# Kernel optimization log

Hardware: AMD Instinct MI355X
Metric: run time of the kernel (lower is better)

## Reference

```python
import math
import jax, jax.numpy as jnp
import numpy as np

# ---- config (from ModelConfig) ----
HIDDEN = 2880
HEAD_DIM = 64
N_HEADS = 64
N_KV = 8
Q_MULT = N_HEADS // N_KV  # 8
SLIDING_WINDOW = 128      # left context; causal windowed attention
ROPE_BASE = 150000.0
ROPE_SCALE = 32.0
NTK_ALPHA = 1.0
NTK_BETA = 32.0
INIT_CTX = 4096
RMS_EPS = 1e-5
SM_SCALE = 1.0 / math.sqrt(HEAD_DIM)
Q_DIM = N_HEADS * HEAD_DIM   # 4096
KV_DIM = N_KV * HEAD_DIM     # 512
QKV_DIM = Q_DIM + 2 * KV_DIM # 5120
B, T = 1, 2048


def _rope_cos_sin(n_tokens):
    """YaRN-scaled rotary cache, per RotaryEmbedding._compute_concentration_and_inv_freq."""
    d_half = HEAD_DIM // 2
    freq = ROPE_BASE ** (jnp.arange(0, HEAD_DIM, 2, dtype=jnp.float32) / HEAD_DIM)
    concentration = 0.1 * math.log(ROPE_SCALE) + 1.0
    low = d_half * math.log(INIT_CTX / (NTK_BETA * 2 * math.pi)) / math.log(ROPE_BASE)
    high = d_half * math.log(INIT_CTX / (NTK_ALPHA * 2 * math.pi)) / math.log(ROPE_BASE)
    interpolation = 1.0 / (ROPE_SCALE * freq)
    extrapolation = 1.0 / freq
    ramp = (jnp.arange(d_half, dtype=jnp.float32) - low) / (high - low)
    mask = 1.0 - jnp.clip(ramp, 0.0, 1.0)
    inv_freq = interpolation * (1.0 - mask) + extrapolation * mask
    pos = jnp.arange(n_tokens, dtype=jnp.float32)
    angles = pos[:, None] * inv_freq[None, :]  # [t, d/2]
    return jnp.cos(angles) * concentration, jnp.sin(angles) * concentration


def _apply_rope(x, cos, sin):
    """Interleaved RoPE (matches _apply_rotary_emb). x: [b, t, ..., d]."""
    shape = x.shape
    n_mid = x.ndim - 3  # dims between token axis and feature axis
    c = cos.reshape((1, shape[1]) + (1,) * n_mid + (shape[-1] // 2,))
    s = sin.reshape((1, shape[1]) + (1,) * n_mid + (shape[-1] // 2,))
    x1 = x[..., ::2]
    x2 = x[..., 1::2]
    o1 = x1 * c - x2 * s
    o2 = x2 * c + x1 * s
    return jnp.stack((o1, o2), axis=-1).reshape(shape)


def _rmsnorm(x, scale):
    t = x.astype(jnp.float32)
    t = t * jax.lax.rsqrt(jnp.mean(t * t, axis=-1, keepdims=True) + RMS_EPS)
    return (t * scale).astype(x.dtype)


def setup_inputs() -> dict:
    key = jax.random.key(0)
    ks = jax.random.split(key, 7)
    x = jax.random.normal(ks[0], (B, T, HIDDEN), dtype=jnp.float32)
    norm_scale = jnp.ones((HIDDEN,), dtype=jnp.float32)
    w_qkv = jax.random.normal(ks[1], (QKV_DIM, HIDDEN), dtype=jnp.float32) * (HIDDEN ** -0.5)
    b_qkv = jax.random.normal(ks[2], (QKV_DIM,), dtype=jnp.float32) * 0.02
    sinks = jax.random.normal(ks[3], (N_HEADS,), dtype=jnp.float32)
    w_out = jax.random.normal(ks[4], (HIDDEN, Q_DIM), dtype=jnp.float32) * (Q_DIM ** -0.5)
    b_out = jax.random.normal(ks[5], (HIDDEN,), dtype=jnp.float32) * 0.02
    return {"x": x, "norm_scale": norm_scale, "w_qkv": w_qkv, "b_qkv": b_qkv,
            "sinks": sinks, "w_out": w_out, "b_out": b_out}


def reference(x, norm_scale, w_qkv, b_qkv, sinks, w_out, b_out):
    b, t, _ = x.shape
    h = _rmsnorm(x, norm_scale)
    qkv = h @ w_qkv.T + b_qkv  # [b, t, 5120]
    q = qkv[..., :Q_DIM].reshape(b, t, N_KV, Q_MULT, HEAD_DIM)
    k = qkv[..., Q_DIM:Q_DIM + KV_DIM].reshape(b, t, N_KV, HEAD_DIM)
    v = qkv[..., Q_DIM + KV_DIM:].reshape(b, t, N_KV, HEAD_DIM)

    cos, sin = _rope_cos_sin(t)
    q = _apply_rope(q, cos, sin)
    k = _apply_rope(k, cos, sin)

    # sliding-window causal attention with sink logits (sdpa windowed path)
    left_ctx = SLIDING_WINDOW
    window = left_ctx + 1
    kp = jnp.pad(k, ((0, 0), (left_ctx, 0), (0, 0), (0, 0)))
    vp = jnp.pad(v, ((0, 0), (left_ctx, 0), (0, 0), (0, 0)))
    gather_idx = jnp.arange(t)[:, None] + jnp.arange(window)[None, :]  # into padded axis
    kwin = kp[:, gather_idx]  # [b, t, w, n_kv, d]
    vwin = vp[:, gather_idx]

    pos = jnp.arange(t)[:, None] + (jnp.arange(window) - left_ctx)[None, :]
    valid = (pos >= 0) & (pos < t)  # [t, w]

    scores = jnp.einsum('bthqd,btwhd->bthqw', q, kwin).astype(jnp.float32) * SM_SCALE
    scores = jnp.where(valid[None, :, None, None, :], scores, -jnp.inf)

    sink = (sinks * math.log(2.0)).reshape(N_KV, Q_MULT)
    sink = jnp.broadcast_to(sink[None, None, :, :, None], (b, t, N_KV, Q_MULT, 1))
    scores = jnp.concatenate([scores, sink], axis=-1)  # [b, t, h, q, w+1]

    w_attn = jax.nn.softmax(scores, axis=-1)[..., :-1].astype(v.dtype)
    attn = jnp.einsum('bthqw,btwhd->bthqd', w_attn, vwin).reshape(b, t, -1)

    out = attn @ w_out.T + b_out
    return x + out
```

## Files before the change

kernel.cpp:

```cpp
#include <hip/hip_runtime.h>
#include <math.h>

typedef unsigned short u16;
typedef unsigned int   u32;
using f32x4  = __attribute__((ext_vector_type(4))) float;
using bf16x8 = __attribute__((ext_vector_type(8))) __bf16;

#define HIDDEN   2880
#define QKVD     5120
#define QD       4096
#define TTOK     2048
#define NKV      8
#define QMULT    8
#define HD       64
#define NPAD     2944

#define PREP_QKV_BLOCKS  14400
#define PREP_RMS_BLOCKS  2048

static __device__ __forceinline__ float bflo(u32 u){ return __uint_as_float(u << 16); }
static __device__ __forceinline__ float bfhi(u32 u){ return __uint_as_float(u & 0xffff0000u); }
static __device__ __forceinline__ u16 f2bf(float f){
    u32 u = __float_as_uint(f);
    u32 r = (u + 0x7fffu + ((u >> 16) & 1u)) >> 16;
    return (u16)r;
}

static __device__ __forceinline__ void glds16(const void* g, void* l) {
    __builtin_amdgcn_global_load_lds(
        (__attribute__((address_space(1))) void*)g,
        (__attribute__((address_space(3))) void*)l,
        16, 0, 0);
}

#define BARB()  __builtin_amdgcn_s_barrier()
#define SB0()   __builtin_amdgcn_sched_barrier(0)
#define LGKM0() do { asm volatile("s_waitcnt lgkmcnt(0)"); SB0(); } while (0)
#define VMW(N)  do { SB0(); asm volatile("s_waitcnt vmcnt(" #N ")"); SB0(); } while (0)

__global__ __launch_bounds__(256) void prep_kernel(const float* __restrict__ w_qkv,
                                                   u16* __restrict__ wqkv_bf,
                                                   const float* __restrict__ x,
                                                   const float* __restrict__ scale,
                                                   u16* __restrict__ h) {
    const int b = blockIdx.x;
    const int tid = threadIdx.x;
    if (b < PREP_QKV_BLOCKS) {
        int i = b * 256 + tid;
        float4 f = ((const float4*)w_qkv)[i];
        ushort4 o;
        o.x = f2bf(f.x); o.y = f2bf(f.y); o.z = f2bf(f.z); o.w = f2bf(f.w);
        ((ushort4*)wqkv_bf)[i] = o;
    } else {
        const int t = b - PREP_QKV_BLOCKS;
        const float4* xr = (const float4*)(x + (long)t * HIDDEN);
        float4 v[3];
        float ss = 0.f;
        #pragma unroll
        for (int it = 0; it < 3; ++it) {
            int i4 = tid + it * 256;
            if (i4 < 720) {
                v[it] = xr[i4];
                ss += v[it].x*v[it].x + v[it].y*v[it].y + v[it].z*v[it].z + v[it].w*v[it].w;
            }
        }
        #pragma unroll
        for (int off = 32; off > 0; off >>= 1) ss += __shfl_down(ss, off);
        __shared__ float red[4];
        if ((tid & 63) == 0) red[tid >> 6] = ss;
        __syncthreads();
        float tot = red[0] + red[1] + red[2] + red[3];
        float rr = rsqrtf(tot * (1.0f / HIDDEN) + 1e-5f);
        ushort4* hr = (ushort4*)(h + (long)t * HIDDEN);
        #pragma unroll
        for (int it = 0; it < 3; ++it) {
            int i4 = tid + it * 256;
            if (i4 < 720) {
                float4 s4 = ((const float4*)scale)[i4];
                ushort4 o;
                o.x = f2bf(v[it].x * rr * s4.x);
                o.y = f2bf(v[it].y * rr * s4.y);
                o.z = f2bf(v[it].z * rr * s4.z);
                o.w = f2bf(v[it].w * rr * s4.w);
                hr[i4] = o;
            }
        }
    }
}


#define LOAD_AQ(MH) do { \
    aq[0][0] = *(const bf16x8*)(aS + (2*(MH)+0)*2048 + off0); \
    aq[0][1] = *(const bf16x8*)(aS + (2*(MH)+0)*2048 + off1); \
    aq[1][0] = *(const bf16x8*)(aS + (2*(MH)+1)*2048 + off0); \
    aq[1][1] = *(const bf16x8*)(aS + (2*(MH)+1)*2048 + off1); \
} while (0)

#define MFMA_Q(MH) do { \
    __builtin_amdgcn_s_setprio(1); \
    _Pragma("unroll") \
    for (int i2_ = 0; i2_ < 2; ++i2_) { \
        _Pragma("unroll") \
        for (int ni_ = 0; ni_ < 4; ++ni_) { \
            acc[2*(MH)+i2_][ni_] = __builtin_amdgcn_mfma_f32_16x16x32_bf16(aq[i2_][0], bq[ni_][0], acc[2*(MH)+i2_][ni_], 0, 0, 0); \
            acc[2*(MH)+i2_][ni_] = __builtin_amdgcn_mfma_f32_16x16x32_bf16(aq[i2_][1], bq[ni_][1], acc[2*(MH)+i2_][ni_], 0, 0, 0); \
        } \
    } \
    __builtin_amdgcn_s_setprio(0); \
} while (0)

__global__ __launch_bounds__(512, 2) void gemm_bt_8ph(const u16* __restrict__ A,
                                                      const u16* __restrict__ B,
                                                      u16* __restrict__ C0,
                                                      int N, int K, int ksplit,
                                                      int blimit, int colmax,
                                                      int nz_gemm,
                                                      const float* __restrict__ wout_src,
                                                      u16* __restrict__ wout_dst) {
    const int tid  = threadIdx.x;

    if ((int)blockIdx.z >= nz_gemm) {
        const long nb = (long)gridDim.x * gridDim.y;
        long bidx = (long)blockIdx.y * gridDim.x + blockIdx.x;
        long i = bidx * 512 + tid;
        const long tot = (long)NPAD * QD / 4;
        const long stride = nb * 512;
        for (; i < tot; i += stride) {
            long idx = i * 4;
            int row = (int)(idx >> 12);
            int col = (int)(idx & 4095);
            ushort4 o;
            if (row < HIDDEN) {
                float4 f = *(const float4*)(wout_src + (long)row * QD + col);
                o.x = f2bf(f.x); o.y = f2bf(f.y); o.z = f2bf(f.z); o.w = f2bf(f.w);
            } else {
                o.x = 0; o.y = 0; o.z = 0; o.w = 0;
            }
            ((ushort4*)wout_dst)[i] = o;
        }
        return;
    }

    extern __shared__ u16 smem[];
    u16* const smA = smem;
    u16* const smB = smem + 3 * 256 * 64;
    const int lane = tid & 63;
    const int wv   = tid >> 6;
    const int wm   = wv >> 2;
    const int wn   = wv & 3;
    const long m0  = (long)blockIdx.y * 256;
    const long n0  = (long)blockIdx.x * 256;
    const int kbase = blockIdx.z * ksplit;
    int krem = K - kbase; if (krem > ksplit) krem = ksplit;
    const int NT   = krem >> 6;
    u16* C = C0 + (size_t)blockIdx.z * ((size_t)TTOK * N);

    const int srow = tid >> 3;
    const int sg8  = ((tid & 7) ^ (srow & 7)) << 3;
    const int fr   = lane & 15;
    const int off0 = ((lane >> 4) << 4) ^ ((lane & 7) << 4);
    const int off1 = off0 ^ 64;
    const char* aR = (const char*)smA + (wm * 128 + fr) * 128;
    const char* bR = (const char*)smB + (wn * 64  + fr) * 128;

    f32x4 acc[8][4];
    #pragma unroll
    for (int i = 0; i < 8; ++i)
        #pragma unroll
        for (int j = 0; j < 4; ++j) acc[i][j] = f32x4{0.f, 0.f, 0.f, 0.f};

    const u16* Asrc = A + (m0 + srow) * (long)K + kbase + sg8;
    auto stageA = [&](int t, int slot) {
        char* dst = (char*)smA + slot * 32768 + (wv * 8) * 128;
        const u16* src = Asrc + t * 64;
        #pragma unroll
        for (int hj = 0; hj < 4; ++hj)
            glds16(src + (size_t)(hj * 64) * K, dst + hj * 64 * 128);
    };
    auto stageB = [&](int t, int h) {
        char* dst = (char*)smB + (t & 1) * 32768 + (h * 128 + wv * 8) * 128;
        #pragma unroll
        for (int j = 0; j < 2; ++j) {
            long r = n0 + h * 128 + j * 64 + srow;
            if (r > blimit) r = blimit;
            glds16(B + (size_t)r * K + kbase + t * 64 + sg8, dst + j * 64 * 128);
        }
    };

    stageA(0, 0);
    stageB(0, 0); stageB(0, 1);
    if (NT > 1) {
        stageA(1, 1); stageB(1, 0); stageB(1, 1);
        VMW(8);
    } else {
        VMW(0);
    }
    BARB();

    int sA = 0;
    for (int t = 0; t < NT; ++t) {
        const char* aS = aR + sA * 32768;
        const char* bS = bR + (t & 1) * 32768;
        int sA2 = sA + 2; if (sA2 >= 3) sA2 -= 3;
        bf16x8 bq[4][2], aq[2][2];
        #pragma unroll
        for (int ni = 0; ni < 4; ++ni) {
            bq[ni][0] = *(const bf16x8*)(bS + ni * 2048 + off0);
            bq[ni][1] = *(const bf16x8*)(bS + ni * 2048 + off1);
        }
        LOAD_AQ(0);
        if (t + 2 < NT) stageA(t + 2, sA2);
        BARB();
        LGKM0();
        MFMA_Q(0);
        BARB();
        LOAD_AQ(1);
        if (t + 2 < NT) stageB(t + 2, 0);
        BARB();
        LGKM0();
        MFMA_Q(1);
        BARB();
        LOAD_AQ(2);
        if (t + 2 < NT) stageB(t + 2, 1);
        BARB();
        LGKM0();
        MFMA_Q(2);
        BARB();
        LOAD_AQ(3);
        BARB();
        LGKM0();
        MFMA_Q(3);
        if (t + 2 < NT)      VMW(8);
        else if (t + 1 < NT) VMW(0);
        BARB();
        sA = (sA == 2) ? 0 : sA + 1;
    }

    const int cr = (lane >> 4) * 4;
    const int cc = lane & 15;
    #pragma unroll
    for (int ni = 0; ni < 4; ++ni) {
        long col = n0 + wn * 64 + ni * 16 + cc;
        if (col < colmax) {
            #pragma unroll
            for (int mi = 0; mi < 8; ++mi) {
                long row = m0 + wm * 128 + mi * 16 + cr;
                #pragma unroll
                for (int r2 = 0; r2 < 4; ++r2)
                    C[(row + r2) * (long)N + col] = f2bf(acc[mi][ni][r2]);
            }
        }
    }
}

__global__ __launch_bounds__(256) void rope_kernel(const u16* __restrict__ p1,
                                                   const float* __restrict__ b_qkv,
                                                   u16* __restrict__ qr,
                                                   u16* __restrict__ kr,
                                                   u16* __restrict__ vr,
                                                   int nsplit) {
    const int t = blockIdx.x;
    const int tid = threadIdx.x;
    __shared__ float cs[32], sn[32];
    if (tid < 32) {
        float fi = (float)tid;
        float freq   = exp2f(17.1946032f * (fi * (1.0f / 32.0f)));
        float interp = 1.0f / (32.0f * freq);
        float extra  = 1.0f / freq;
        float ramp   = (fi - 8.0927802f) * (1.0f / (17.3980220f - 8.0927802f));
        float rc     = fminf(fmaxf(ramp, 0.0f), 1.0f);
        float invf   = interp * rc + extra * (1.0f - rc);
        float ang    = (float)t * invf;
        cs[tid] = cosf(ang) * 1.3465736f;
        sn[tid] = sinf(ang) * 1.3465736f;
    }
    __syncthreads();
    const u16* rowA = p1 + (long)t * QKVD;
    auto pair = [&](int col) -> float2 {
        float2 bb = *(const float2*)(b_qkv + col);
        float a = bb.x, b = bb.y;
        for (int s = 0; s < nsplit; ++s) {
            u32 u = *(const u32*)(rowA + (size_t)s * TTOK * QKVD + col);
            a += bflo(u); b += bfhi(u);
        }
        return make_float2(a, b);
    };
    for (int p = tid; p < 2048; p += 256) {
        int hd2 = p >> 5, i = p & 31;
        float2 ab = pair(hd2 * 64 + 2 * i);
        float o1 = ab.x * cs[i] - ab.y * sn[i];
        float o2 = ab.y * cs[i] + ab.x * sn[i];
        *(u32*)(qr + (long)t * QD + hd2 * 64 + 2 * i) = (u32)f2bf(o1) | ((u32)f2bf(o2) << 16);
    }
    {
        int kv = tid >> 5, i = tid & 31;
        float2 ab = pair(QD + kv * 64 + 2 * i);
        float o1 = ab.x * cs[i] - ab.y * sn[i];
        float o2 = ab.y * cs[i] + ab.x * sn[i];
        *(u32*)(kr + ((long)kv * TTOK + t) * HD + 2 * i) = (u32)f2bf(o1) | ((u32)f2bf(o2) << 16);
    }
    {
        int kv = tid >> 5, d2 = tid & 31;
        float2 ab = pair(QD + 512 + kv * 64 + 2 * d2);
        *(u32*)(vr + ((long)kv * TTOK + t) * HD + 2 * d2) = (u32)f2bf(ab.x) | ((u32)f2bf(ab.y) << 16);
    }
}

__global__ __launch_bounds__(256, 2) void attn_kernel(const u16* __restrict__ qr,
                                                      const u16* __restrict__ kr,
                                                      const u16* __restrict__ vr,
                                                      const float* __restrict__ sinks,
                                                      u16* __restrict__ o) {
    const int t0  = blockIdx.x * 16;
    const int h   = blockIdx.y;
    const int qhg = blockIdx.z;
    const int tid = threadIdx.x;
    const int lane = tid & 63, wv = tid >> 6;
    __shared__ __align__(16) u16 ks[144][72];
    __shared__ __align__(16) u16 Vt[64][168];
    __shared__ __align__(16) u16 P [4][16][168];
    const u16* kb = kr + (long)h * TTOK * HD;
    const u16* vb = vr + (long)h * TTOK * HD;

    #pragma unroll
    for (int i = 0; i < 5; ++i) {
        int idx = i * 256 + tid;
        if (idx < 144 * 8) {
            int rr = idx >> 3, c = idx & 7;
            int tk = t0 - 128 + rr;
            int tks = tk < 0 ? 0 : tk;
            *(uint4*)&ks[rr][c * 8] = *(const uint4*)(kb + (long)tks * HD + c * 8);
        }
    }
    #pragma unroll
    for (int c4 = 0; c4 < 8; ++c4) {
        if (tid < 144) {
            int tk = t0 - 128 + tid;
            int tks = tk < 0 ? 0 : tk;
            uint4 v4 = *(const uint4*)(vb + (long)tks * HD + c4 * 8);
            int d0 = c4 * 8;
            Vt[d0+0][tid] = (u16)(v4.x & 0xffff); Vt[d0+1][tid] = (u16)(v4.x >> 16);
            Vt[d0+2][tid] = (u16)(v4.y & 0xffff); Vt[d0+3][tid] = (u16)(v4.y >> 16);
            Vt[d0+4][tid] = (u16)(v4.z & 0xffff); Vt[d0+5][tid] = (u16)(v4.z >> 16);
            Vt[d0+6][tid] = (u16)(v4.w & 0xffff); Vt[d0+7][tid] = (u16)(v4.w >> 16);
        }
    }
    if (tid < 128) {
        *(uint4*)&Vt[tid >> 1][144 + (tid & 1) * 8] = uint4{0, 0, 0, 0};
    }
    if (lane < 32) {
        *(uint4*)&P[wv][lane >> 1][144 + (lane & 1) * 8] = uint4{0, 0, 0, 0};
    }
    __syncthreads();

    const int qh   = qhg * 4 + wv;
    const int head = h * QMULT + qh;
    const int fr = lane & 15, fk = (lane >> 4) * 8;
    const int cr = (lane >> 4) * 4;

    const u16* qrow = qr + (long)(t0 + fr) * QD + head * HD;
    bf16x8 qf0 = *(const bf16x8*)(qrow + fk);
    bf16x8 qf1 = *(const bf16x8*)(qrow + 32 + fk);

    const int kmin = 128 - t0;
    float lsum[4] = {0.f, 0.f, 0.f, 0.f};

    for (int nt = 0; nt < 9; ++nt) {
        bf16x8 b0 = *(const bf16x8*)&ks[nt * 16 + fr][fk];
        bf16x8 b1 = *(const bf16x8*)&ks[nt * 16 + fr][32 + fk];
        f32x4 s = f32x4{0.f, 0.f, 0.f, 0.f};
        s = __builtin_amdgcn_mfma_f32_16x16x32_bf16(qf0, b0, s, 0, 0, 0);
        s = __builtin_amdgcn_mfma_f32_16x16x32_bf16(qf1, b1, s, 0, 0, 0);
        const int kk = nt * 16 + fr;
        #pragma unroll
        for (int r = 0; r < 4; ++r) {
            int row = cr + r;
            bool valid = (kk >= row) && (kk <= row + 128) && (kk >= kmin);
            float p = valid ? __expf(s[r] * 0.125f) : 0.0f;
            lsum[r] += p;
            P[wv][row][kk] = f2bf(p);
        }
    }

    f32x4 oacc[4];
    #pragma unroll
    for (int dt = 0; dt < 4; ++dt) oacc[dt] = f32x4{0.f, 0.f, 0.f, 0.f};
    #pragma unroll
    for (int k5 = 0; k5 < 5; ++k5) {
        const int k0 = k5 * 32;
        bf16x8 pa = *(const bf16x8*)&P[wv][fr][k0 + fk];
        #pragma unroll
        for (int dt = 0; dt < 4; ++dt) {
            bf16x8 vf = *(const bf16x8*)&Vt[dt * 16 + fr][k0 + fk];
            oacc[dt] = __builtin_amdgcn_mfma_f32_16x16x32_bf16(pa, vf, oacc[dt], 0, 0, 0);
        }
    }

    #pragma unroll
    for (int r = 0; r < 4; ++r) {
        float v = lsum[r];
        v += __shfl_xor(v, 1);
        v += __shfl_xor(v, 2);
        v += __shfl_xor(v, 4);
        v += __shfl_xor(v, 8);
        lsum[r] = v;
    }
    const float sk = exp2f(sinks[head]);
    float inv[4];
    #pragma unroll
    for (int r = 0; r < 4; ++r) inv[r] = 1.0f / (lsum[r] + sk);

    #pragma unroll
    for (int dt = 0; dt < 4; ++dt) {
        #pragma unroll
        for (int r = 0; r < 4; ++r) {
            o[(long)(t0 + cr + r) * QD + head * HD + dt * 16 + fr] = f2bf(oacc[dt][r] * inv[r]);
        }
    }
}

__global__ __launch_bounds__(256) void reduce2_kernel(const u16* __restrict__ p2a,
                                                      const u16* __restrict__ p2b,
                                                      const float* __restrict__ x,
                                                      const float* __restrict__ b_out,
                                                      float* __restrict__ out) {
    const int row = blockIdx.y;
    const int c4 = blockIdx.x * 256 + threadIdx.x;
    if (c4 >= 720) return;
    const int col = c4 * 4;
    ushort4 ua = *(const ushort4*)(p2a + (long)row * NPAD + col);
    ushort4 ub = *(const ushort4*)(p2b + (long)row * NPAD + col);
    float4 xv = *(const float4*)(x + (long)row * HIDDEN + col);
    float4 bv = *(const float4*)(b_out + col);
    float4 o;
    o.x = xv.x + bv.x + __uint_as_float((u32)ua.x << 16) + __uint_as_float((u32)ub.x << 16);
    o.y = xv.y + bv.y + __uint_as_float((u32)ua.y << 16) + __uint_as_float((u32)ub.y << 16);
    o.z = xv.z + bv.z + __uint_as_float((u32)ua.z << 16) + __uint_as_float((u32)ub.z << 16);
    o.w = xv.w + bv.w + __uint_as_float((u32)ua.w << 16) + __uint_as_float((u32)ub.w << 16);
    *(float4*)(out + (long)row * HIDDEN + col) = o;
}

extern "C" void kernel_launch(void* const* d_in, const int* in_sizes, int n_in,
                              void* d_out, int out_size, void* d_ws, size_t ws_size,
                              hipStream_t stream) {
    const float* x      = (const float*)d_in[0];
    const float* nscale = (const float*)d_in[1];
    const float* w_qkv  = (const float*)d_in[2];
    const float* b_qkv  = (const float*)d_in[3];
    const float* sinks  = (const float*)d_in[4];
    const float* w_out  = (const float*)d_in[5];
    const float* b_out  = (const float*)d_in[6];
    float* out = (float*)d_out;

    static int smem_set = 0;
    if (!smem_set) {
        hipFuncSetAttribute((const void*)gemm_bt_8ph,
                            hipFuncAttributeMaxDynamicSharedMemorySize, 163840);
        smem_set = 1;
    }

    char* ws = (char*)d_ws;
    size_t off = 0;
    auto alloc = [&](size_t bytes) { void* p = ws + off; off += (bytes + 255) & ~(size_t)255; return p; };
    const size_t p1_bytes  = (size_t)TTOK * QKVD * 2;
    const size_t p2_bytes  = (size_t)2 * TTOK * NPAD * 2;
    u16* wqkv_bf = (u16*)alloc((size_t)QKVD * HIDDEN * 2);
    u16* wout_bf = (u16*)alloc((size_t)NPAD * QD * 2);
    u16* h       = (u16*)alloc((size_t)TTOK * HIDDEN * 2);
    u16* p1      = (u16*)alloc(p1_bytes > p2_bytes ? p1_bytes : p2_bytes);
    u16* qrot    = (u16*)alloc((size_t)TTOK * QD * 2);
    u16* attn = wqkv_bf;
    u16* krot = wqkv_bf + (size_t)TTOK * QD;
    u16* vrot = krot + (size_t)NKV * TTOK * HD;
    u16* p2   = p1;

    prep_kernel<<<PREP_QKV_BLOCKS + PREP_RMS_BLOCKS, 256, 0, stream>>>(
        w_qkv, wqkv_bf, x, nscale, h);
    gemm_bt_8ph<<<dim3(QKVD / 256, TTOK / 256, 2), 512, 163840, stream>>>(
        h, wqkv_bf, p1, QKVD, HIDDEN, HIDDEN, QKVD - 1, QKVD, 1, w_out, wout_bf);
    rope_kernel<<<TTOK, 256, 0, stream>>>(p1, b_qkv, qrot, krot, vrot, 1);
    attn_kernel<<<dim3(TTOK / 16, NKV, 2), 256, 0, stream>>>(qrot, krot, vrot, sinks, attn);
    gemm_bt_8ph<<<dim3((NPAD + 255) / 256, TTOK / 256, 2), 512, 163840, stream>>>(
        attn, wout_bf, p2, NPAD, QD, QD / 2, NPAD - 1, NPAD, 2, nullptr, nullptr);
    reduce2_kernel<<<dim3(3, TTOK), 256, 0, stream>>>(
        p2, p2 + (size_t)TTOK * NPAD, x, b_out, out);
}
```

Measured before the change: 337.0 us.

## Replace 256x256 eight-phase GEMM with simpler 128x256 double-buffered kernel

Replaces the hand-scheduled 256x256-tile GEMM (triple-buffered A, 64-wide K steps, many barriers and priority hints, 160KB dynamic LDS) with a 128x256 tile, 32-wide K step, double-buffered static-LDS GEMM that issues one syncthreads per step. Occupancy is raised to 4 blocks per CU and the grid has twice as many M tiles, aiming for more parallelism and latency hiding. The trade-off is less data reuse per tile, more LDS traffic per FLOP, loss of the fine-grained load/MFMA interleaving, and a barrier per short K step.

```diff
diff --git a/kernel.cpp b/kernel.cpp
--- a/kernel.cpp
+++ b/kernel.cpp
@@ -32,11 +32,6 @@
         (__attribute__((address_space(3))) void*)l,
         16, 0, 0);
 }
-
-#define BARB()  __builtin_amdgcn_s_barrier()
-#define SB0()   __builtin_amdgcn_sched_barrier(0)
-#define LGKM0() do { asm volatile("s_waitcnt lgkmcnt(0)"); SB0(); } while (0)
-#define VMW(N)  do { SB0(); asm volatile("s_waitcnt vmcnt(" #N ")"); SB0(); } while (0)
 
 __global__ __launch_bounds__(256) void prep_kernel(const float* __restrict__ w_qkv,
                                                    u16* __restrict__ wqkv_bf,
@@ -88,35 +83,14 @@
     }
 }
 
-
-#define LOAD_AQ(MH) do { \
-    aq[0][0] = *(const bf16x8*)(aS + (2*(MH)+0)*2048 + off0); \
-    aq[0][1] = *(const bf16x8*)(aS + (2*(MH)+0)*2048 + off1); \
-    aq[1][0] = *(const bf16x8*)(aS + (2*(MH)+1)*2048 + off0); \
-    aq[1][1] = *(const bf16x8*)(aS + (2*(MH)+1)*2048 + off1); \
-} while (0)
-
-#define MFMA_Q(MH) do { \
-    __builtin_amdgcn_s_setprio(1); \
-    _Pragma("unroll") \
-    for (int i2_ = 0; i2_ < 2; ++i2_) { \
-        _Pragma("unroll") \
-        for (int ni_ = 0; ni_ < 4; ++ni_) { \
-            acc[2*(MH)+i2_][ni_] = __builtin_amdgcn_mfma_f32_16x16x32_bf16(aq[i2_][0], bq[ni_][0], acc[2*(MH)+i2_][ni_], 0, 0, 0); \
-            acc[2*(MH)+i2_][ni_] = __builtin_amdgcn_mfma_f32_16x16x32_bf16(aq[i2_][1], bq[ni_][1], acc[2*(MH)+i2_][ni_], 0, 0, 0); \
-        } \
-    } \
-    __builtin_amdgcn_s_setprio(0); \
-} while (0)
-
-__global__ __launch_bounds__(512, 2) void gemm_bt_8ph(const u16* __restrict__ A,
-                                                      const u16* __restrict__ B,
-                                                      u16* __restrict__ C0,
-                                                      int N, int K, int ksplit,
-                                                      int blimit, int colmax,
-                                                      int nz_gemm,
-                                                      const float* __restrict__ wout_src,
-                                                      u16* __restrict__ wout_dst) {
+__global__ __launch_bounds__(512, 4) void gemm_bt(const u16* __restrict__ A,
+                                                  const u16* __restrict__ B,
+                                                  u16* __restrict__ C0,
+                                                  int N, int K, int ksplit,
+                                                  int blimit, int colmax,
+                                                  int nz_gemm,
+                                                  const float* __restrict__ wout_src,
+                                                  u16* __restrict__ wout_dst) {
     const int tid  = threadIdx.x;
 
     if ((int)blockIdx.z >= nz_gemm) {
@@ -141,113 +115,75 @@
         return;
     }
 
-    extern __shared__ u16 smem[];
-    u16* const smA = smem;
-    u16* const smB = smem + 3 * 256 * 64;
+    __shared__ __align__(16) u16 smA[2][128 * 32];
+    __shared__ __align__(16) u16 smB[2][256 * 32];
     const int lane = tid & 63;
     const int wv   = tid >> 6;
     const int wm   = wv >> 2;
     const int wn   = wv & 3;
-    const long m0  = (long)blockIdx.y * 256;
+    const long m0  = (long)blockIdx.y * 128;
     const long n0  = (long)blockIdx.x * 256;
     const int kbase = blockIdx.z * ksplit;
     int krem = K - kbase; if (krem > ksplit) krem = ksplit;
-    const int NT   = krem >> 6;
+    const int NT   = krem >> 5;
     u16* C = C0 + (size_t)blockIdx.z * ((size_t)TTOK * N);
 
-    const int srow = tid >> 3;
-    const int sg8  = ((tid & 7) ^ (srow & 7)) << 3;
+    const int srow = tid >> 2;
+    const int sg8  = ((tid & 3) ^ ((tid >> 2) & 3)) << 3;
+    const u16* Asrc = A + (m0 + srow) * (long)K + kbase + sg8;
     const int fr   = lane & 15;
-    const int off0 = ((lane >> 4) << 4) ^ ((lane & 7) << 4);
-    const int off1 = off0 ^ 64;
-    const char* aR = (const char*)smA + (wm * 128 + fr) * 128;
-    const char* bR = (const char*)smB + (wn * 64  + fr) * 128;
-
-    f32x4 acc[8][4];
-    #pragma unroll
-    for (int i = 0; i < 8; ++i)
+    const int offr = (((lane >> 4) ^ (lane & 3)) << 4);
+    const char* aR = (const char*)smA + (wm * 64 + fr) * 64 + offr;
+    const char* bR = (const char*)smB + (wn * 64 + fr) * 64 + offr;
+
+    f32x4 acc[4][4];
+    #pragma unroll
+    for (int i = 0; i < 4; ++i)
         #pragma unroll
         for (int j = 0; j < 4; ++j) acc[i][j] = f32x4{0.f, 0.f, 0.f, 0.f};
 
-    const u16* Asrc = A + (m0 + srow) * (long)K + kbase + sg8;
-    auto stageA = [&](int t, int slot) {
-        char* dst = (char*)smA + slot * 32768 + (wv * 8) * 128;
-        const u16* src = Asrc + t * 64;
-        #pragma unroll
-        for (int hj = 0; hj < 4; ++hj)
-            glds16(src + (size_t)(hj * 64) * K, dst + hj * 64 * 128);
+    auto stage = [&](int t, int buf) {
+        glds16(Asrc + t * 32, (char*)smA + buf * 8192 + wv * 1024);
+        #pragma unroll
+        for (int j = 0; j < 2; ++j) {
+            long r = n0 + j * 128 + srow;
+            if (r > blimit) r = blimit;
+            glds16(B + (size_t)r * K + kbase + t * 32 + sg8,
+                   (char*)smB + buf * 16384 + j * 8192 + wv * 1024);
+        }
     };
-    auto stageB = [&](int t, int h) {
-        char* dst = (char*)smB + (t & 1) * 32768 + (h * 128 + wv * 8) * 128;
-        #pragma unroll
-        for (int j = 0; j < 2; ++j) {
-            long r = n0 + h * 128 + j * 64 + srow;
-            if (r > blimit) r = blimit;
-            glds16(B + (size_t)r * K + kbase + t * 64 + sg8, dst + j * 64 * 128);
-        }
-    };
-
-    stageA(0, 0);
-    stageB(0, 0); stageB(0, 1);
-    if (NT > 1) {
-        stageA(1, 1); stageB(1, 0); stageB(1, 1);
-        VMW(8);
-    } else {
-        VMW(0);
-    }
-    BARB();
-
-    int sA = 0;
-    for (int t = 0; t < NT; ++t) {
-        const char* aS = aR + sA * 32768;
-        const char* bS = bR + (t & 1) * 32768;
-        int sA2 = sA + 2; if (sA2 >= 3) sA2 -= 3;
-        bf16x8 bq[4][2], aq[2][2];
-        #pragma unroll
-        for (int ni = 0; ni < 4; ++ni) {
-            bq[ni][0] = *(const bf16x8*)(bS + ni * 2048 + off0);
-            bq[ni][1] = *(const bf16x8*)(bS + ni * 2048 + off1);
-        }
-        LOAD_AQ(0);
-        if (t + 2 < NT) stageA(t + 2, sA2);
-        BARB();
-        LGKM0();
-        MFMA_Q(0);
-        BARB();
-        LOAD_AQ(1);
-        if (t + 2 < NT) stageB(t + 2, 0);
-        BARB();
-        LGKM0();
-        MFMA_Q(1);
-        BARB();
-        LOAD_AQ(2);
-        if (t + 2 < NT) stageB(t + 2, 1);
-        BARB();
-        LGKM0();
-        MFMA_Q(2);
-        BARB();
-        LOAD_AQ(3);
-        BARB();
-        LGKM0();
-        MFMA_Q(3);
-        if (t + 2 < NT)      VMW(8);
-        else if (t + 1 < NT) VMW(0);
-        BARB();
-        sA = (sA == 2) ? 0 : sA + 1;
+
+    stage(0, 0);
+    int ib = 0;
+    for (int t = 0; t < NT; ++t, ib ^= 1) {
+        __syncthreads();
+        if (t + 1 < NT) stage(t + 1, ib ^ 1);
+        bf16x8 af[4], bf[4];
+        #pragma unroll
+        for (int mi = 0; mi < 4; ++mi)
+            af[mi] = *(const bf16x8*)(aR + ib * 8192 + mi * 1024);
+        #pragma unroll
+        for (int nf = 0; nf < 4; ++nf)
+            bf[nf] = *(const bf16x8*)(bR + ib * 16384 + nf * 1024);
+        #pragma unroll
+        for (int mi = 0; mi < 4; ++mi)
+            #pragma unroll
+            for (int nf = 0; nf < 4; ++nf)
+                acc[mi][nf] = __builtin_amdgcn_mfma_f32_16x16x32_bf16(af[mi], bf[nf], acc[mi][nf], 0, 0, 0);
     }
 
     const int cr = (lane >> 4) * 4;
     const int cc = lane & 15;
     #pragma unroll
-    for (int ni = 0; ni < 4; ++ni) {
-        long col = n0 + wn * 64 + ni * 16 + cc;
+    for (int nf = 0; nf < 4; ++nf) {
+        long col = n0 + wn * 64 + nf * 16 + cc;
         if (col < colmax) {
             #pragma unroll
-            for (int mi = 0; mi < 8; ++mi) {
-                long row = m0 + wm * 128 + mi * 16 + cr;
+            for (int mi = 0; mi < 4; ++mi) {
+                long row = m0 + wm * 64 + mi * 16 + cr;
                 #pragma unroll
                 for (int r2 = 0; r2 < 4; ++r2)
-                    C[(row + r2) * (long)N + col] = f2bf(acc[mi][ni][r2]);
+                    C[(row + r2) * (long)N + col] = f2bf(acc[mi][nf][r2]);
             }
         }
     }
@@ -452,13 +388,6 @@
     const float* b_out  = (const float*)d_in[6];
     float* out = (float*)d_out;
 
-    static int smem_set = 0;
-    if (!smem_set) {
-        hipFuncSetAttribute((const void*)gemm_bt_8ph,
-                            hipFuncAttributeMaxDynamicSharedMemorySize, 163840);
-        smem_set = 1;
-    }
-
     char* ws = (char*)d_ws;
     size_t off = 0;
     auto alloc = [&](size_t bytes) { void* p = ws + off; off += (bytes + 255) & ~(size_t)255; return p; };
@@ -476,11 +405,11 @@
 
     prep_kernel<<<PREP_QKV_BLOCKS + PREP_RMS_BLOCKS, 256, 0, stream>>>(
         w_qkv, wqkv_bf, x, nscale, h);
-    gemm_bt_8ph<<<dim3(QKVD / 256, TTOK / 256, 2), 512, 163840, stream>>>(
+    gemm_bt<<<dim3(QKVD / 256, TTOK / 128, 2), 512, 0, stream>>>(
         h, wqkv_bf, p1, QKVD, HIDDEN, HIDDEN, QKVD - 1, QKVD, 1, w_out, wout_bf);
     rope_kernel<<<TTOK, 256, 0, stream>>>(p1, b_qkv, qrot, krot, vrot, 1);
     attn_kernel<<<dim3(TTOK / 16, NKV, 2), 256, 0, stream>>>(qrot, krot, vrot, sinks, attn);
-    gemm_bt_8ph<<<dim3((NPAD + 255) / 256, TTOK / 256, 2), 512, 163840, stream>>>(
+    gemm_bt<<<dim3((NPAD + 255) / 256, TTOK / 128, 2), 512, 0, stream>>>(
         attn, wout_bf, p2, NPAD, QD, QD / 2, NPAD - 1, NPAD, 2, nullptr, nullptr);
     reduce2_kernel<<<dim3(3, TTOK), 256, 0, stream>>>(
         p2, p2 + (size_t)TTOK * NPAD, x, b_out, out);
```

Result: slower. 353.0 us (+4.7%).
